# Kernel optimization log

Hardware: AMD Instinct MI355X
Metric: run time of the kernel (lower is better)

## Reference

```python
import jax, jax.numpy as jnp
import numpy as np

B, N, D, H = 4, 2048, 1024, 16
DH = D // H  # 64


def setup_inputs() -> dict:
    key = jax.random.key(0)
    k1, k2, k3 = jax.random.split(key, 3)
    x = jax.random.normal(k1, (B, N, D), dtype=jnp.float32)
    w_qkv = jax.random.normal(k2, (D, 3 * D), dtype=jnp.float32) * (1.0 / np.sqrt(D))
    b_qkv = jnp.zeros((3 * D,), dtype=jnp.float32)
    w_o = jax.random.normal(k3, (D, D), dtype=jnp.float32) * (1.0 / np.sqrt(D))
    b_o = jnp.zeros((D,), dtype=jnp.float32)
    return {"x": x, "w_qkv": w_qkv, "b_qkv": b_qkv, "w_o": w_o, "b_o": b_o}


def reference(x, w_qkv, b_qkv, w_o, b_o):
    b, n, d = x.shape
    qkv = x @ w_qkv + b_qkv                         # [B, N, 3D]
    q, k, v = jnp.split(qkv, 3, axis=-1)
    # [B, H, N, DH]
    q = q.reshape(b, n, H, DH).transpose(0, 2, 1, 3)
    k = k.reshape(b, n, H, DH).transpose(0, 2, 1, 3)
    v = v.reshape(b, n, H, DH).transpose(0, 2, 1, 3)
    scale = 1.0 / np.sqrt(DH)
    att = jnp.einsum("bhqd,bhkd->bhqk", q, k) * scale  # [B, H, N, N]
    causal = jnp.tril(jnp.ones((n, n), dtype=bool))
    att = jnp.where(causal[None, None, :, :], att, -jnp.inf)
    att = jax.nn.softmax(att, axis=-1)
    y = jnp.einsum("bhqk,bhkd->bhqd", att, v)          # [B, H, N, DH]
    y = y.transpose(0, 2, 1, 3).reshape(b, n, d)
    return y @ w_o + b_o
```

## Files before the change

kernel.cpp:

```cpp
#include <hip/hip_runtime.h>

typedef unsigned short u16;
typedef unsigned short u16x4 __attribute__((ext_vector_type(4), may_alias));
typedef unsigned short u16x8 __attribute__((ext_vector_type(8), may_alias));
typedef __bf16 bf16x8 __attribute__((ext_vector_type(8), may_alias));
typedef float f32x4 __attribute__((ext_vector_type(4), may_alias));

typedef __attribute__((address_space(1))) void gvoid_t;
typedef __attribute__((address_space(3))) void lvoid_t;

__device__ __forceinline__ void gld16(const void* g, void* l) {
    __builtin_amdgcn_global_load_lds((gvoid_t*)g, (lvoid_t*)l, 16, 0, 0);
}

__device__ __forceinline__ u16 f2bf(float f) {
    unsigned u = __builtin_bit_cast(unsigned, f);
    u += 0x7fffu + ((u >> 16) & 1u);
    return (u16)(u >> 16);
}

__device__ __forceinline__ unsigned cvt_pk_bf16(float lo, float hi) {
    unsigned r;
    asm("v_cvt_pk_bf16_f32 %0, %1, %2" : "=v"(r) : "v"(lo), "v"(hi));
    return r;
}

#define KSCALE 0.18033688011112042f

__global__ __launch_bounds__(256) void cvt_f32_bf16_k(const float* __restrict__ in,
                                                      u16* __restrict__ out, int n8) {
    int i = blockIdx.x * 256 + threadIdx.x;
    if (i >= n8) return;
    float4 a = reinterpret_cast<const float4*>(in)[2 * i];
    float4 c = reinterpret_cast<const float4*>(in)[2 * i + 1];
    u16x8 o;
    o[0] = f2bf(a.x); o[1] = f2bf(a.y); o[2] = f2bf(a.z); o[3] = f2bf(a.w);
    o[4] = f2bf(c.x); o[5] = f2bf(c.y); o[6] = f2bf(c.z); o[7] = f2bf(c.w);
    reinterpret_cast<u16x8*>(out)[i] = o;
}

__global__ __launch_bounds__(256) void tr_f32_bf16_k(const float* __restrict__ in,
                                                     u16* __restrict__ out, int R, int C) {
    __shared__ u16 t[64][73];
    int tc = C >> 6;
    int r0 = (blockIdx.x / tc) << 6, c0 = (blockIdx.x % tc) << 6;
    int lr = threadIdx.x >> 2;
    int lc = (threadIdx.x & 3) << 4;
    const float* src = in + (size_t)(r0 + lr) * C + c0 + lc;
#pragma unroll
    for (int j = 0; j < 16; j += 4) {
        float4 v = *reinterpret_cast<const float4*>(src + j);
        t[lr][lc + j + 0] = f2bf(v.x);
        t[lr][lc + j + 1] = f2bf(v.y);
        t[lr][lc + j + 2] = f2bf(v.z);
        t[lr][lc + j + 3] = f2bf(v.w);
    }
    __syncthreads();
    u16x8 o0, o1;
#pragma unroll
    for (int j = 0; j < 8; j++) { o0[j] = t[lc + j][lr]; o1[j] = t[lc + 8 + j][lr]; }
    u16* dst = out + (size_t)(c0 + lr) * R + r0 + lc;
    *reinterpret_cast<u16x8*>(dst) = o0;
    *reinterpret_cast<u16x8*>(dst + 8) = o1;
}

template <int MODE>
__global__ __launch_bounds__(256, 4) void gemm_bt_k(const u16* __restrict__ A,
                                                    const u16* __restrict__ Bt,
                                                    const float* __restrict__ bias,
                                                    u16* __restrict__ Qp, u16* __restrict__ Kp,
                                                    u16* __restrict__ Vt,
                                                    float* __restrict__ Cf,
                                                    int M, int N, int K) {
    __shared__ u16 As[128 * 64];
    __shared__ u16 Bs[128 * 64];
    const int tid = threadIdx.x;
    const int l = tid & 63, w = tid >> 6;
    const int wm = w >> 1, wn = w & 1;
    const int l16 = l & 15, lg = l >> 4;
    const int tc = N >> 7;
    const int bm = blockIdx.x / tc, bn = blockIdx.x % tc;
    const u16* Ab = A + (size_t)(bm << 7) * K;
    const u16* Bb = Bt + (size_t)(bn << 7) * K;

    f32x4 acc[4][4];
#pragma unroll
    for (int mi = 0; mi < 4; mi++)
#pragma unroll
        for (int ni = 0; ni < 4; ni++)
#pragma unroll
            for (int q = 0; q < 4; q++) acc[mi][ni][q] = 0.f;

    auto stage = [&](int k0) {
#pragma unroll
        for (int i = 0; i < 4; i++) {
            int s = tid + (i << 8);
            int ub = ((i << 8) + (w << 6)) << 3;
            gld16(Ab + (size_t)(s >> 3) * K + k0 + ((s & 7) << 3), &As[ub]);
            gld16(Bb + (size_t)(s >> 3) * K + k0 + ((s & 7) << 3), &Bs[ub]);
        }
    };

    stage(0);
    for (int k0 = 0; k0 < K; k0 += 64) {
        __syncthreads();
#pragma unroll
        for (int kk = 0; kk < 2; kk++) {
            bf16x8 af[4], bfr[4];
#pragma unroll
            for (int mi = 0; mi < 4; mi++)
                af[mi] = *reinterpret_cast<const bf16x8*>(
                    &As[((wm << 6) + (mi << 4) + l16) * 64 + (kk << 5) + (lg << 3)]);
#pragma unroll
            for (int ni = 0; ni < 4; ni++)
                bfr[ni] = *reinterpret_cast<const bf16x8*>(
                    &Bs[((wn << 6) + (ni << 4) + l16) * 64 + (kk << 5) + (lg << 3)]);
#pragma unroll
            for (int mi = 0; mi < 4; mi++)
#pragma unroll
                for (int ni = 0; ni < 4; ni++)
                    acc[mi][ni] = __builtin_amdgcn_mfma_f32_16x16x32_bf16(af[mi], bfr[ni], acc[mi][ni], 0, 0, 0);
        }
        __syncthreads();
        if (k0 + 64 < K) stage(k0 + 64);
    }

    const int rb = (bm << 7) + (wm << 6), cb = (bn << 7) + (wn << 6);
    if constexpr (MODE == 0) {
        const int sec = cb >> 10;
#pragma unroll
        for (int ni = 0; ni < 4; ni++) {
            const int col = cb + (ni << 4) + l16;
            const float bb = bias[col];
            const int d = col & 1023, h = d >> 6, dh = d & 63;
#pragma unroll
            for (int mi = 0; mi < 4; mi++) {
                const int row0 = rb + (mi << 4) + (lg << 2);
                const int bidx = row0 >> 11, n0 = row0 & 2047;
                const size_t base = (size_t)(bidx * 16 + h) * 131072;
                if (sec == 0) {
#pragma unroll
                    for (int r = 0; r < 4; r++)
                        Qp[base + (size_t)(n0 + r) * 64 + dh] = f2bf(acc[mi][ni][r] + bb);
                } else if (sec == 1) {
#pragma unroll
                    for (int r = 0; r < 4; r++)
                        Kp[base + (size_t)(n0 + r) * 64 + dh] = f2bf((acc[mi][ni][r] + bb) * KSCALE);
                } else {
                    u16x4 pk;
#pragma unroll
                    for (int r = 0; r < 4; r++) pk[r] = f2bf(acc[mi][ni][r] + bb);
                    *reinterpret_cast<u16x4*>(&Vt[base + (size_t)dh * 2048 + n0]) = pk;
                }
            }
        }
    } else {
#pragma unroll
        for (int ni = 0; ni < 4; ni++) {
            const int col = cb + (ni << 4) + l16;
            const float bb = bias[col];
#pragma unroll
            for (int mi = 0; mi < 4; mi++)
#pragma unroll
                for (int r = 0; r < 4; r++) {
                    const int row = rb + (mi << 4) + (lg << 2) + r;
                    Cf[(size_t)row * N + col] = acc[mi][ni][r] + bb;
                }
        }
    }
}

__global__ __launch_bounds__(256, 3) void attn_k(const u16* __restrict__ Qp,
                                                 const u16* __restrict__ Kp,
                                                 const u16* __restrict__ Vt,
                                                 u16* __restrict__ Y) {
    __shared__ u16 Ks[2][64 * 64];
    __shared__ u16 Vs[2][64 * 64];
    __shared__ u16 P_lds[4][16 * 72];
    const int tid = threadIdx.x;
    const int l = tid & 63, w = tid >> 6;
    const int l16 = l & 15, lg = l >> 4;
    const int swz = (blockIdx.x & 7) * 256 + (blockIdx.x >> 3);
    const int bh = swz >> 5;
    const int QT = 31 - (swz & 31);
    const int nt = QT + 1;
    const int b = bh >> 4, h = bh & 15;
    const u16* Qb = Qp + (size_t)bh * 131072;
    const u16* Kb = Kp + (size_t)bh * 131072;
    const u16* Vb = Vt + (size_t)bh * 131072;
    u16* pl = &P_lds[w][0];

    const int qrow0 = QT * 64 + w * 16;
    bf16x8 qf[2];
#pragma unroll
    for (int kk = 0; kk < 2; kk++)
        qf[kk] = *reinterpret_cast<const bf16x8*>(
            Qb + (size_t)(qrow0 + l16) * 64 + kk * 32 + lg * 8);

    f32x4 o[4];
    float m_s = -1e30f, l_s = 0.f;
#pragma unroll
    for (int n = 0; n < 4; n++)
#pragma unroll
        for (int r = 0; r < 4; r++) o[n][r] = 0.f;

    const int lr = l >> 3;
    const int sslot = (l & 7) ^ lr;
    const int r0 = w * 16;
    auto stage = [&](int buf, int kv0) {
        gld16(Kb + (size_t)(kv0 + r0 + lr) * 64 + sslot * 8,       &Ks[buf][r0 * 64]);
        gld16(Kb + (size_t)(kv0 + r0 + 8 + lr) * 64 + sslot * 8,   &Ks[buf][(r0 + 8) * 64]);
        gld16(Vb + (size_t)(r0 + lr) * 2048 + kv0 + sslot * 8,     &Vs[buf][r0 * 64]);
        gld16(Vb + (size_t)(r0 + 8 + lr) * 2048 + kv0 + sslot * 8, &Vs[buf][(r0 + 8) * 64]);
    };

    stage(0, 0);
    int cur = 0;
    const int xs = l16 & 7;
#pragma unroll 1
    for (int it = 0; it < nt; it++) {
        __syncthreads();
        if (it + 1 < nt) stage(cur ^ 1, (it + 1) * 64);
        float s4[4][4];
#pragma unroll
        for (int t = 0; t < 4; t++) {
            f32x4 s;
            s[0] = s[1] = s[2] = s[3] = 0.f;
#pragma unroll
            for (int kk = 0; kk < 2; kk++) {
                bf16x8 kf = *reinterpret_cast<const bf16x8*>(
                    &Ks[cur][(t * 16 + l16) * 64 + ((kk * 4 + lg) ^ xs) * 8]);
                s = __builtin_amdgcn_mfma_f32_16x16x32_bf16(kf, qf[kk], s, 0, 0, 0);
            }
#pragma unroll
            for (int r = 0; r < 4; r++) s4[t][r] = s[r];
        }
        if (it == nt - 1) {
            const int qg = w * 16 + l16;
            const int kvb = lg * 4;
#pragma unroll
            for (int t = 0; t < 4; t++)
#pragma unroll
                for (int r = 0; r < 4; r++)
                    if (kvb + t * 16 + r > qg) s4[t][r] = -1e30f;
        }
        float mt[4];
#pragma unroll
        for (int t = 0; t < 4; t++)
            mt[t] = fmaxf(fmaxf(s4[t][0], s4[t][1]), fmaxf(s4[t][2], s4[t][3]));
        float mx = fmaxf(fmaxf(mt[0], mt[1]), fmaxf(mt[2], mt[3]));
        mx = fmaxf(mx, __shfl_xor(mx, 16, 64));
        mx = fmaxf(mx, __shfl_xor(mx, 32, 64));
        if (__any(mx - m_s > 8.0f)) {
            float mn = fmaxf(m_s, mx);
            float al = __builtin_amdgcn_exp2f(m_s - mn);
            m_s = mn;
            l_s *= al;
#pragma unroll
            for (int r = 0; r < 4; r++) {
                float ar = __shfl(al, lg * 4 + r, 64);
#pragma unroll
                for (int n = 0; n < 4; n++) o[n][r] *= ar;
            }
        }
#pragma unroll
        for (int t = 0; t < 4; t++)
#pragma unroll
            for (int r = 0; r < 4; r++)
                s4[t][r] = __builtin_amdgcn_exp2f(s4[t][r] - m_s);
        float st[4];
#pragma unroll
        for (int t = 0; t < 4; t++)
            st[t] = (s4[t][0] + s4[t][1]) + (s4[t][2] + s4[t][3]);
        float sm = (st[0] + st[1]) + (st[2] + st[3]);
        sm += __shfl_xor(sm, 16, 64);
        sm += __shfl_xor(sm, 32, 64);
        l_s += sm;
#pragma unroll
        for (int t = 0; t < 4; t++) {
            uint2 pk;
            pk.x = cvt_pk_bf16(s4[t][0], s4[t][1]);
            pk.y = cvt_pk_bf16(s4[t][2], s4[t][3]);
            *reinterpret_cast<uint2*>(pl + l16 * 72 + t * 16 + lg * 4) = pk;
        }
        bf16x8 pa[2];
#pragma unroll
        for (int kk2 = 0; kk2 < 2; kk2++)
            pa[kk2] = *reinterpret_cast<const bf16x8*>(pl + l16 * 72 + kk2 * 32 + lg * 8);
#pragma unroll
        for (int n = 0; n < 4; n++) {
            bf16x8 v0 = *reinterpret_cast<const bf16x8*>(
                &Vs[cur][(n * 16 + l16) * 64 + ((0 * 4 + lg) ^ xs) * 8]);
            bf16x8 v1 = *reinterpret_cast<const bf16x8*>(
                &Vs[cur][(n * 16 + l16) * 64 + ((1 * 4 + lg) ^ xs) * 8]);
            o[n] = __builtin_amdgcn_mfma_f32_16x16x32_bf16(pa[0], v0, o[n], 0, 0, 0);
            o[n] = __builtin_amdgcn_mfma_f32_16x16x32_bf16(pa[1], v1, o[n], 0, 0, 0);
        }
        cur ^= 1;
    }
#pragma unroll
    for (int r = 0; r < 4; r++) {
        const float li = __shfl(l_s, lg * 4 + r, 64);
        const float inv = 1.0f / li;
        const size_t row = (size_t)(b * 2048 + qrow0 + lg * 4 + r);
#pragma unroll
        for (int n = 0; n < 4; n++)
            Y[row * 1024 + h * 64 + n * 16 + l16] = f2bf(o[n][r] * inv);
    }
}

extern "C" void kernel_launch(void* const* d_in, const int* in_sizes, int n_in,
                              void* d_out, int out_size, void* d_ws, size_t ws_size,
                              hipStream_t stream) {
    const float* x     = (const float*)d_in[0];
    const float* w_qkv = (const float*)d_in[1];
    const float* b_qkv = (const float*)d_in[2];
    const float* w_o   = (const float*)d_in[3];
    const float* b_o   = (const float*)d_in[4];
    float* out = (float*)d_out;

    u16* ws  = (u16*)d_ws;
    u16* xb  = ws;
    u16* wqT = ws + 8388608;
    u16* woT = ws + 11534336;
    u16* Qp  = ws + 12582912;
    u16* Kp  = ws + 20971520;
    u16* Vt  = ws + 29360128;

    cvt_f32_bf16_k<<<4096, 256, 0, stream>>>(x, xb, 1048576);
    tr_f32_bf16_k<<<768, 256, 0, stream>>>(w_qkv, wqT, 1024, 3072);
    tr_f32_bf16_k<<<256, 256, 0, stream>>>(w_o, woT, 1024, 1024);
    gemm_bt_k<0><<<1536, 256, 0, stream>>>(xb, wqT, b_qkv, Qp, Kp, Vt, nullptr, 8192, 3072, 1024);
    attn_k<<<2048, 256, 0, stream>>>(Qp, Kp, Vt, xb);
    gemm_bt_k<1><<<512, 256, 0, stream>>>(xb, woT, b_o, nullptr, nullptr, nullptr, out, 8192, 1024, 1024);
}
```

Baseline: 201.0 us.

## Single-buffer attention K/V tiles and raise occupancy bounds with explicit vmcnt waits

The attention kernel drops its double-buffered K/V LDS tiles and uses a single buffer. The next tile is now loaded only after a second barrier at the end of each iteration. Launch bounds rise to 6 blocks per CU for both the GEMM and attention kernels, and explicit s_waitcnt vmcnt(0) plus scheduling barriers are added before the loop barriers. The intent is to cut LDS and register use so more waves can hide latency, but load/compute overlap inside a block is lost and register pressure under the tighter bound may cause spills.

Result: slower. 225.4 us (+12.1%).

```diff
diff --git a/kernel.cpp b/kernel.cpp
--- a/kernel.cpp
+++ b/kernel.cpp
@@ -65,7 +65,7 @@
 }
 
 template <int MODE>
-__global__ __launch_bounds__(256, 4) void gemm_bt_k(const u16* __restrict__ A,
+__global__ __launch_bounds__(256, 6) void gemm_bt_k(const u16* __restrict__ A,
                                                     const u16* __restrict__ Bt,
                                                     const float* __restrict__ bias,
                                                     u16* __restrict__ Qp, u16* __restrict__ Kp,
@@ -103,6 +103,8 @@
 
     stage(0);
     for (int k0 = 0; k0 < K; k0 += 64) {
+        asm volatile("s_waitcnt vmcnt(0)" ::: "memory");
+        __builtin_amdgcn_sched_barrier(0);
         __syncthreads();
 #pragma unroll
         for (int kk = 0; kk < 2; kk++) {
@@ -170,12 +172,12 @@
     }
 }
 
-__global__ __launch_bounds__(256, 3) void attn_k(const u16* __restrict__ Qp,
+__global__ __launch_bounds__(256, 6) void attn_k(const u16* __restrict__ Qp,
                                                  const u16* __restrict__ Kp,
                                                  const u16* __restrict__ Vt,
                                                  u16* __restrict__ Y) {
-    __shared__ u16 Ks[2][64 * 64];
-    __shared__ u16 Vs[2][64 * 64];
+    __shared__ u16 Ks[64 * 64];
+    __shared__ u16 Vs[64 * 64];
     __shared__ u16 P_lds[4][16 * 72];
     const int tid = threadIdx.x;
     const int l = tid & 63, w = tid >> 6;
@@ -207,20 +209,20 @@
     const int lr = l >> 3;
     const int sslot = (l & 7) ^ lr;
     const int r0 = w * 16;
-    auto stage = [&](int buf, int kv0) {
-        gld16(Kb + (size_t)(kv0 + r0 + lr) * 64 + sslot * 8,       &Ks[buf][r0 * 64]);
-        gld16(Kb + (size_t)(kv0 + r0 + 8 + lr) * 64 + sslot * 8,   &Ks[buf][(r0 + 8) * 64]);
-        gld16(Vb + (size_t)(r0 + lr) * 2048 + kv0 + sslot * 8,     &Vs[buf][r0 * 64]);
-        gld16(Vb + (size_t)(r0 + 8 + lr) * 2048 + kv0 + sslot * 8, &Vs[buf][(r0 + 8) * 64]);
+    auto stage = [&](int kv0) {
+        gld16(Kb + (size_t)(kv0 + r0 + lr) * 64 + sslot * 8,       &Ks[r0 * 64]);
+        gld16(Kb + (size_t)(kv0 + r0 + 8 + lr) * 64 + sslot * 8,   &Ks[(r0 + 8) * 64]);
+        gld16(Vb + (size_t)(r0 + lr) * 2048 + kv0 + sslot * 8,     &Vs[r0 * 64]);
+        gld16(Vb + (size_t)(r0 + 8 + lr) * 2048 + kv0 + sslot * 8, &Vs[(r0 + 8) * 64]);
     };
 
-    stage(0, 0);
-    int cur = 0;
+    stage(0);
     const int xs = l16 & 7;
 #pragma unroll 1
     for (int it = 0; it < nt; it++) {
+        asm volatile("s_waitcnt vmcnt(0)" ::: "memory");
+        __builtin_amdgcn_sched_barrier(0);
         __syncthreads();
-        if (it + 1 < nt) stage(cur ^ 1, (it + 1) * 64);
         float s4[4][4];
 #pragma unroll
         for (int t = 0; t < 4; t++) {
@@ -229,7 +231,7 @@
 #pragma unroll
             for (int kk = 0; kk < 2; kk++) {
                 bf16x8 kf = *reinterpret_cast<const bf16x8*>(
-                    &Ks[cur][(t * 16 + l16) * 64 + ((kk * 4 + lg) ^ xs) * 8]);
+                    &Ks[(t * 16 + l16) * 64 + ((kk * 4 + lg) ^ xs) * 8]);
                 s = __builtin_amdgcn_mfma_f32_16x16x32_bf16(kf, qf[kk], s, 0, 0, 0);
             }
 #pragma unroll
@@ -290,13 +292,14 @@
 #pragma unroll
         for (int n = 0; n < 4; n++) {
             bf16x8 v0 = *reinterpret_cast<const bf16x8*>(
-                &Vs[cur][(n * 16 + l16) * 64 + ((0 * 4 + lg) ^ xs) * 8]);
+                &Vs[(n * 16 + l16) * 64 + ((0 * 4 + lg) ^ xs) * 8]);
             bf16x8 v1 = *reinterpret_cast<const bf16x8*>(
-                &Vs[cur][(n * 16 + l16) * 64 + ((1 * 4 + lg) ^ xs) * 8]);
+                &Vs[(n * 16 + l16) * 64 + ((1 * 4 + lg) ^ xs) * 8]);
             o[n] = __builtin_amdgcn_mfma_f32_16x16x32_bf16(pa[0], v0, o[n], 0, 0, 0);
             o[n] = __builtin_amdgcn_mfma_f32_16x16x32_bf16(pa[1], v1, o[n], 0, 0, 0);
         }
-        cur ^= 1;
+        __syncthreads();
+        if (it + 1 < nt) stage((it + 1) * 64);
     }
 #pragma unroll
     for (int r = 0; r < 4; r++) {
```
